# Kernel optimization log

Hardware: AMD Instinct MI355X
Metric: run time of the kernel (lower is better)

## Reference

```python
import jax, jax.numpy as jnp
import numpy as np

B, N, F, H, D = 4096, 14, 768, 1, 768  # batch, num_diseases, feature_dim, num_heads, hidden_dim
L = 3  # number of GAT layers


def setup_inputs() -> dict:
    key = jax.random.key(0)
    ks = jax.random.split(key, 8)
    features = jax.random.normal(ks[0], (B, N, F), dtype=jnp.float32)
    # random adjacency mask; ensure nonzero diagonal so no row is fully masked
    mask = (jax.random.uniform(ks[1], (B, N, N)) > 0.3).astype(jnp.float32)
    adj = jnp.maximum(mask, jnp.eye(N, dtype=jnp.float32))
    W_emb = jax.random.normal(ks[2], (F, D), dtype=jnp.float32) / np.sqrt(F)
    b_emb = jnp.zeros((D,), dtype=jnp.float32)
    gat_W = jax.random.normal(ks[3], (L, D, H * D), dtype=jnp.float32) / np.sqrt(D)
    gat_a = jax.random.normal(ks[4], (L, 2 * D, H), dtype=jnp.float32) / np.sqrt(2 * D)
    W_out = jax.random.normal(ks[5], (H * D, F), dtype=jnp.float32) / np.sqrt(H * D)
    b_out = jnp.zeros((F,), dtype=jnp.float32)
    return dict(features=features, adj=adj, W_emb=W_emb, b_emb=b_emb,
                gat_W=gat_W, gat_a=gat_a, W_out=W_out, b_out=b_out)


def _gat_layer(x, adj, W, a):
    # x: [B, N, D], W: [D, H*D], a: [2D, H]
    Bm, Nn = x.shape[0], x.shape[1]
    Wh = (x @ W).reshape(Bm, Nn, H, D)
    # e[b,i,j,h] = Wh[b,i,h] . a[:D,h] + Wh[b,j,h] . a[D:,h]  (concat attention, un-materialized)
    a_i, a_j = a[:D], a[D:]
    ei = jnp.einsum('bnhd,dh->bnh', Wh, a_i)
    ej = jnp.einsum('bnhd,dh->bnh', Wh, a_j)
    e = ei[:, :, None, :] + ej[:, None, :, :]  # [B, N, N, H]
    e = jnp.where(adj[..., None] > 0, e, jnp.float32(-1e30))  # masked_fill(-inf)
    attn = jax.nn.softmax(e, axis=2)  # softmax over j (dim=2), matches torch
    h = jnp.einsum('bijh,bjhd->bihd', attn, Wh)  # attention-weighted aggregation
    return h.reshape(Bm, Nn, H * D), attn  # concat=True output


def reference(features, adj, W_emb, b_emb, gat_W, gat_a, W_out, b_out):
    # dropout layers are identity at inference
    x = features @ W_emb + b_emb  # disease_embedding
    attns = []
    for l in range(L):
        x, attn = _gat_layer(x, adj, gat_W[l], gat_a[l])
        attns.append(attn)
        if l < L - 1:
            x = jax.nn.elu(x)
    out = x @ W_out + b_out  # output_proj
    return (out, attns[0], attns[1], attns[2])
```

## Files before the change

### kernel.cpp

```cpp
#include <hip/hip_runtime.h>

typedef unsigned short u16;
typedef float f32x16 __attribute__((ext_vector_type(16)));
typedef short bf16x8 __attribute__((ext_vector_type(8)));
typedef unsigned short u16x8 __attribute__((ext_vector_type(8)));

#define ND 768
#define KD 768

__device__ __forceinline__ float bf2f(u16 u) {
    union { unsigned i; float f; } v; v.i = ((unsigned)u) << 16; return v.f;
}
__device__ __forceinline__ u16 f2bf(float f) {
    union { float f; unsigned u; } x; x.f = f;
    unsigned r = x.u + 0x7fffu + ((x.u >> 16) & 1u);
    return (u16)(r >> 16);
}
__device__ __forceinline__ void async16(const void* g, void* l) {
    __builtin_amdgcn_global_load_lds((const __attribute__((address_space(1))) void*)g,
                                     (__attribute__((address_space(3))) void*)l, 16, 0, 0);
}

__global__ __launch_bounds__(256) void conv_w(const float* __restrict__ W_emb,
                                              const float* __restrict__ gat_W,
                                              const float* __restrict__ W_out,
                                              u16* __restrict__ Wt)
{
    __shared__ float lds[64][65];
    const int m  = blockIdx.x / 144;
    const int r  = blockIdx.x % 144;
    const int tr = r / 12;
    const int tc = r % 12;
    const float* src = (m == 0) ? W_emb : (m <= 3) ? (gat_W + (size_t)(m - 1) * 589824) : W_out;
    const int c  = threadIdx.x & 63;
    const int w4 = threadIdx.x >> 6;
    #pragma unroll
    for (int i = 0; i < 16; ++i) {
        int kk = i * 4 + w4;
        lds[kk][c] = src[(size_t)(tr * 64 + kk) * 768 + tc * 64 + c];
    }
    __syncthreads();
    u16* dst = Wt + (size_t)m * 589824;
    #pragma unroll
    for (int i = 0; i < 16; ++i) {
        int nn = i * 4 + w4;
        dst[(size_t)(tc * 64 + nn) * 768 + tr * 64 + c] = f2bf(lds[c][nn]);
    }
}

__global__ __launch_bounds__(256) void conv_w2(const float* __restrict__ src0,
                                               u16* __restrict__ dst0)
{
    __shared__ float lds[64][65];
    const int m  = blockIdx.x / 144;
    const int r  = blockIdx.x % 144;
    const int tr = r / 12;
    const int tc = r % 12;
    const float* src = src0 + (size_t)m * 589824;
    u16* dst = dst0 + (size_t)m * 589824;
    const int c  = threadIdx.x & 63;
    const int w4 = threadIdx.x >> 6;
    #pragma unroll
    for (int i = 0; i < 16; ++i) {
        int kk = i * 4 + w4;
        lds[kk][c] = src[(size_t)(tr * 64 + kk) * 768 + tc * 64 + c];
    }
    __syncthreads();
    #pragma unroll
    for (int i = 0; i < 16; ++i) {
        int nn = i * 4 + w4;
        dst[(size_t)(tc * 64 + nn) * 768 + tr * 64 + c] = f2bf(lds[c][nn]);
    }
}

__global__ __launch_bounds__(256) void conv_x(const float4* __restrict__ in,
                                              u16* __restrict__ outp, int n4)
{
    for (int i = blockIdx.x * 256 + threadIdx.x; i < n4; i += gridDim.x * 256) {
        float4 v = in[i];
        union { u16 s[4]; uint2 u; } o;
        o.s[0] = f2bf(v.x); o.s[1] = f2bf(v.y); o.s[2] = f2bf(v.z); o.s[3] = f2bf(v.w);
        ((uint2*)outp)[i] = o.u;
    }
}

__global__ __launch_bounds__(256) void prep_vecs(const float* __restrict__ W3,
                                                 const float* __restrict__ ga2,
                                                 const float* __restrict__ be,
                                                 const u16* __restrict__ Wt1,
                                                 float* __restrict__ w3ai,
                                                 float* __restrict__ w3aj,
                                                 float* __restrict__ bfus)
{
    int d = blockIdx.x * 256 + threadIdx.x;
    if (d >= 768) return;
    const float* row = W3 + (size_t)d * 768;
    float ai = 0.f, aj = 0.f;
    for (int n = 0; n < 768; ++n) { float w = row[n]; ai += w * ga2[n]; aj += w * ga2[768 + n]; }
    w3ai[d] = ai; w3aj[d] = aj;
    const u16* wt = Wt1 + (size_t)d * 768;
    float bf = 0.f;
    for (int j = 0; j < 768; ++j) bf += be[j] * bf2f(wt[j]);
    bfus[d] = bf;
}

template<bool F32OUT, bool SWZ>
__global__ __launch_bounds__(256) void gemm_bt(const u16* __restrict__ A,
                                               const u16* __restrict__ Bt,
                                               const u16* __restrict__ Bt2,
                                               const float* __restrict__ bias,
                                               void* __restrict__ Cout)
{
    __shared__ u16 lds3[3][2][4096];
    const int tid  = threadIdx.x;
    const int lane = tid & 63;
    const int wvb  = tid & ~63;
    const int wm   = ((tid >> 7) & 1) * 64;
    const int wn   = ((tid >> 6) & 1) * 64;
    const int wg = blockIdx.x;
    const int id = SWZ ? ((wg & 7) * 336 + (wg >> 3)) : wg;
    const int tn = (id % 6) * 128;
    const int tm = (id / 6) * 128;
    const u16* BtU = (Bt2 != nullptr && tm >= 768) ? Bt2 : Bt;

    f32x16 acc[2][2] = {};

    const int r31 = lane & 31;
    const int l5  = lane >> 5;
    const int key = (r31 >> 1) & 3;

    const int row0 = tid >> 2;
    const int kc0  = (((tid & 3) ^ ((tid >> 3) & 3)) << 3);
    const u16* aSrc = A   + (size_t)(tm + row0) * KD + kc0;
    const u16* bSrc = BtU + (size_t)(tn + row0) * KD + kc0;

    #define STAGE(b, ks_) { const int k0 = (ks_) * 32;                       \
        async16(aSrc + k0,                   &lds3[b][0][wvb * 8]);          \
        async16(aSrc + (size_t)64 * KD + k0, &lds3[b][0][(256 + wvb) * 8]);  \
        async16(bSrc + k0,                   &lds3[b][1][wvb * 8]);          \
        async16(bSrc + (size_t)64 * KD + k0, &lds3[b][1][(256 + wvb) * 8]); }

    STAGE(0, 0);
    STAGE(1, 1);

    #pragma unroll 3
    for (int ks = 0; ks < KD / 32; ++ks) {
        const int cur = ks % 3;
        if (ks < KD / 32 - 1)
            asm volatile("s_waitcnt vmcnt(4)" ::: "memory");
        else
            asm volatile("s_waitcnt vmcnt(0)" ::: "memory");
        __builtin_amdgcn_s_barrier();
        asm volatile("" ::: "memory");
        if (ks + 2 < KD / 32) STAGE((ks + 2) % 3, ks + 2);

        const u16* As = lds3[cur][0];
        const u16* Bs = lds3[cur][1];
        bf16x8 af[2][2], bf[2][2];
        #pragma unroll
        for (int fr = 0; fr < 2; ++fr)
            #pragma unroll
            for (int ka = 0; ka < 2; ++ka) {
                int chA = ((ka * 2 + l5) ^ key) << 3;
                af[fr][ka] = *(const bf16x8*)&As[(wm + fr * 32 + r31) * 32 + chA];
                bf[fr][ka] = *(const bf16x8*)&Bs[(wn + fr * 32 + r31) * 32 + chA];
            }
        #pragma unroll
        for (int fr = 0; fr < 2; ++fr)
            #pragma unroll
            for (int fc = 0; fc < 2; ++fc)
                #pragma unroll
                for (int ka = 0; ka < 2; ++ka)
                    acc[fr][fc] = __builtin_amdgcn_mfma_f32_32x32x16_bf16(
                        af[fr][ka], bf[fc][ka], acc[fr][fc], 0, 0, 0);
    }
    #undef STAGE

    #pragma unroll
    for (int fc = 0; fc < 2; ++fc) {
        int col = tn + wn + fc * 32 + r31;
        float bv = bias ? bias[col] : 0.0f;
        #pragma unroll
        for (int fr = 0; fr < 2; ++fr) {
            int rowb = tm + wm + fr * 32 + 4 * l5;
            #pragma unroll
            for (int reg = 0; reg < 16; ++reg) {
                int row = rowb + (reg & 3) + 8 * (reg >> 2);
                float v = acc[fr][fc][reg] + bv;
                if (F32OUT)
                    ((float*)Cout)[(size_t)row * ND + col] = v;
                else
                    ((u16*)Cout)[(size_t)row * ND + col] = f2bf(v);
            }
        }
    }
}

template<bool ELU, bool DOTS>
__global__ __launch_bounds__(256) void gat_mix(const u16* __restrict__ Wh,
                                               const float* __restrict__ adj,
                                               const float* __restrict__ avec,
                                               float* __restrict__ attn_out,
                                               u16* __restrict__ Xout,
                                               const float* __restrict__ w3ai,
                                               const float* __restrict__ w3aj,
                                               float* __restrict__ eiOut,
                                               float* __restrict__ ejOut)
{
    __shared__ u16 wh[14 * 768];
    __shared__ float s_ei[14], s_ej[14];
    __shared__ float s_attn[196];
    __shared__ float s_dots[14][2];
    const int b = blockIdx.x;
    const int tid = threadIdx.x;
    const u16* whb = Wh + (size_t)b * 10752;

    if (DOTS && tid < 28) ((float*)s_dots)[tid] = 0.f;
    for (int c = tid; c < 1344; c += 256)
        ((uint4*)wh)[c] = ((const uint4*)whb)[c];
    __syncthreads();

    if (tid < 224) {
        const int i = tid >> 4, l = tid & 15;
        float ai = 0.f, aj = 0.f;
        #pragma unroll
        for (int c = 0; c < 6; ++c) {
            int d = c * 128 + l * 8;
            u16x8 v  = *(const u16x8*)&wh[i * 768 + d];
            float4 x0 = *(const float4*)&avec[d];
            float4 x1 = *(const float4*)&avec[d + 4];
            float4 y0 = *(const float4*)&avec[768 + d];
            float4 y1 = *(const float4*)&avec[768 + d + 4];
            float w0 = bf2f(v[0]), w1 = bf2f(v[1]), w2 = bf2f(v[2]), w3 = bf2f(v[3]);
            float w4 = bf2f(v[4]), w5 = bf2f(v[5]), w6 = bf2f(v[6]), w7 = bf2f(v[7]);
            ai += w0*x0.x + w1*x0.y + w2*x0.z + w3*x0.w + w4*x1.x + w5*x1.y + w6*x1.z + w7*x1.w;
            aj += w0*y0.x + w1*y0.y + w2*y0.z + w3*y0.w + w4*y1.x + w5*y1.y + w6*y1.z + w7*y1.w;
        }
        #pragma unroll
        for (int off = 8; off; off >>= 1) {
            ai += __shfl_xor(ai, off);
            aj += __shfl_xor(aj, off);
        }
        if (l == 0) { s_ei[i] = ai; s_ej[i] = aj; }
    }
    __syncthreads();

    if (tid < 14) {
        const int i = tid;
        float e[14];
        float mx = -3.0e38f;
        #pragma unroll
        for (int j = 0; j < 14; ++j) {
            float ev = (adj[(size_t)b * 196 + i * 14 + j] > 0.f) ? (s_ei[i] + s_ej[j]) : -1.0e30f;
            e[j] = ev; mx = fmaxf(mx, ev);
        }
        float sum = 0.f;
        #pragma unroll
        for (int j = 0; j < 14; ++j) { float pp = __expf(e[j] - mx); e[j] = pp; sum += pp; }
        float inv = 1.0f / sum;
        #pragma unroll
        for (int j = 0; j < 14; ++j) s_attn[i * 14 + j] = e[j] * inv;
    }
    __syncthreads();

    if (tid < 196) attn_out[(size_t)b * 196 + tid] = s_attn[tid];

    for (int pp = tid; pp < 14 * 48; pp += 256) {
        const int i  = pp / 48;
        const int d0 = (pp % 48) * 16;
        float acc[16] = {};
        #pragma unroll
        for (int j = 0; j < 14; ++j) {
            float aw = s_attn[i * 14 + j];
            u16x8 wv0 = *(const u16x8*)&wh[j * 768 + d0];
            u16x8 wv1 = *(const u16x8*)&wh[j * 768 + d0 + 8];
            #pragma unroll
            for (int qq = 0; qq < 8; ++qq) {
                acc[qq]     += aw * bf2f(wv0[qq]);
                acc[8 + qq] += aw * bf2f(wv1[qq]);
            }
        }
        float pi = 0.f, pj = 0.f;
        union { u16 s[16]; uint4 u[2]; } o;
        #pragma unroll
        for (int qq = 0; qq < 16; ++qq) {
            float v = acc[qq];
            if (ELU && v < 0.f) v = __expf(v) - 1.0f;
            if (DOTS) { pi += v * w3ai[d0 + qq]; pj += v * w3aj[d0 + qq]; }
            o.s[qq] = f2bf(v);
        }
        if (DOTS) {
            atomicAdd(&s_dots[i][0], pi);
            atomicAdd(&s_dots[i][1], pj);
        }
        *(uint4*)&Xout[(size_t)b * 10752 + i * 768 + d0]     = o.u[0];
        *(uint4*)&Xout[(size_t)b * 10752 + i * 768 + d0 + 8] = o.u[1];
    }
    if (DOTS) {
        __syncthreads();
        if (tid < 14) {
            eiOut[(size_t)b * 14 + tid] = s_dots[tid][0];
            ejOut[(size_t)b * 14 + tid] = s_dots[tid][1];
        }
    }
}

__global__ __launch_bounds__(256) void gat_out(const u16* __restrict__ Z,
                                               const float* __restrict__ adj,
                                               const float* __restrict__ eiG,
                                               const float* __restrict__ ejG,
                                               const float* __restrict__ b_out,
                                               float* __restrict__ attn_out,
                                               float* __restrict__ outp)
{
    __shared__ u16 wh[14 * 768];
    __shared__ float s_attn[196];
    const int b = blockIdx.x;
    const int tid = threadIdx.x;
    const u16* zb = Z + (size_t)b * 10752;

    for (int c = tid; c < 1344; c += 256)
        ((uint4*)wh)[c] = ((const uint4*)zb)[c];

    if (tid < 14) {
        const int i = tid;
        float ei = eiG[(size_t)b * 14 + i];
        float e[14];
        float mx = -3.0e38f;
        #pragma unroll
        for (int j = 0; j < 14; ++j) {
            float ev = (adj[(size_t)b * 196 + i * 14 + j] > 0.f)
                           ? (ei + ejG[(size_t)b * 14 + j]) : -1.0e30f;
            e[j] = ev; mx = fmaxf(mx, ev);
        }
        float sum = 0.f;
        #pragma unroll
        for (int j = 0; j < 14; ++j) { float pp = __expf(e[j] - mx); e[j] = pp; sum += pp; }
        float inv = 1.0f / sum;
        #pragma unroll
        for (int j = 0; j < 14; ++j) s_attn[i * 14 + j] = e[j] * inv;
    }
    __syncthreads();

    if (tid < 196) attn_out[(size_t)b * 196 + tid] = s_attn[tid];

    for (int pp = tid; pp < 14 * 48; pp += 256) {
        const int i  = pp / 48;
        const int d0 = (pp % 48) * 16;
        float acc[16];
        #pragma unroll
        for (int qq = 0; qq < 16; ++qq) acc[qq] = b_out[d0 + qq];
        #pragma unroll
        for (int j = 0; j < 14; ++j) {
            float aw = s_attn[i * 14 + j];
            u16x8 wv0 = *(const u16x8*)&wh[j * 768 + d0];
            u16x8 wv1 = *(const u16x8*)&wh[j * 768 + d0 + 8];
            #pragma unroll
            for (int qq = 0; qq < 8; ++qq) {
                acc[qq]     += aw * bf2f(wv0[qq]);
                acc[8 + qq] += aw * bf2f(wv1[qq]);
            }
        }
        float* dst = &outp[(size_t)b * 10752 + i * 768 + d0];
        *(float4*)(dst)      = *(float4*)&acc[0];
        *(float4*)(dst + 4)  = *(float4*)&acc[4];
        *(float4*)(dst + 8)  = *(float4*)&acc[8];
        *(float4*)(dst + 12) = *(float4*)&acc[12];
    }
}

extern "C" void kernel_launch(void* const* d_in, const int* in_sizes, int n_in,
                              void* d_out, int out_size, void* d_ws, size_t ws_size,
                              hipStream_t stream)
{
    const float* features = (const float*)d_in[0];
    const float* adj      = (const float*)d_in[1];
    const float* W_emb    = (const float*)d_in[2];
    const float* b_emb    = (const float*)d_in[3];
    const float* gat_W    = (const float*)d_in[4];
    const float* gat_a    = (const float*)d_in[5];
    const float* W_out    = (const float*)d_in[6];
    const float* b_out    = (const float*)d_in[7];
    float* out = (float*)d_out;

    u16* Wh = (u16*)d_ws;
    u16* Wt = Wh + 44040192;
    float* scr  = (float*)(Wt + 7 * 589824);
    float* w3ai = scr + 1179648;
    float* w3aj = w3ai + 768;
    float* bfus = w3aj + 768;
    float* eiG  = bfus + 768;
    float* ejG  = eiG + 57344;
    u16* H0 = (u16*)d_out;
    u16* H1 = H0 + 44040192;
    u16* WeW3 = H1;
    float* attn0 = out + 44040192;
    float* attn1 = attn0 + 802816;
    float* attn2 = attn1 + 802816;

    conv_w<<<dim3(720), 256, 0, stream>>>(W_emb, gat_W, W_out, Wt);
    conv_x<<<dim3(4096), 256, 0, stream>>>((const float4*)features, H0, 11010048);
    conv_x<<<dim3(576), 256, 0, stream>>>((const float4*)W_emb, WeW3, 147456);
    conv_x<<<dim3(576), 256, 0, stream>>>((const float4*)(gat_W + 2 * 589824), WeW3 + 589824, 147456);
    prep_vecs<<<dim3(3), 256, 0, stream>>>(gat_W + 2 * 589824, gat_a + 2 * 1536, b_emb,
                                           Wt + 589824, w3ai, w3aj, bfus);
    gemm_bt<true, false><<<dim3(72), 256, 0, stream>>>(
        WeW3, Wt + 1 * 589824, Wt + 4 * 589824, nullptr, scr);
    conv_w2<<<dim3(288), 256, 0, stream>>>(scr, Wt + 5 * 589824);

    dim3 gg(2688);
    gemm_bt<false, true><<<gg, 256, 0, stream>>>(
        H0, Wt + 5 * 589824, nullptr, bfus, Wh);
    gat_mix<true, false><<<dim3(4096), 256, 0, stream>>>(Wh, adj, gat_a, attn0, H1,
                                                         nullptr, nullptr, nullptr, nullptr);
    gemm_bt<false, true><<<gg, 256, 0, stream>>>(
        H1, Wt + 2 * 589824, nullptr, nullptr, Wh);
    gat_mix<true, true><<<dim3(4096), 256, 0, stream>>>(Wh, adj, gat_a + 1536, attn1, H0,
                                                        w3ai, w3aj, eiG, ejG);
    gemm_bt<false, true><<<gg, 256, 0, stream>>>(
        H0, Wt + 6 * 589824, nullptr, nullptr, Wh);
    gat_out<<<dim3(4096), 256, 0, stream>>>(Wh, adj, eiG, ejG, b_out, attn2, out);
}
```

Before: 638.6 us.

## Merge weight prep kernels, parallelize prep_vecs, emit fused weights pre-transposed

Merges the weight transposes, the bf16 casts of W_emb and W3, and the features cast into one mega_prep launch. prep_vecs now gives one wavefront per output row with a shuffle reduction instead of one serial thread per row. The small fused-weight GEMM swaps operand roles so its bf16 output is already transposed, which removes the fp32 scratch buffer and the conv_w2 transpose. These cut launch count and serial prep latency, at the cost of a more branchy prep kernel and a skipped W_emb transpose slot.

```diff
diff --git a/kernel.cpp b/kernel.cpp
--- a/kernel.cpp
+++ b/kernel.cpp
@@ -21,91 +21,89 @@
                                      (__attribute__((address_space(3))) void*)l, 16, 0, 0);
 }
 
-__global__ __launch_bounds__(256) void conv_w(const float* __restrict__ W_emb,
-                                              const float* __restrict__ gat_W,
-                                              const float* __restrict__ W_out,
-                                              u16* __restrict__ Wt)
+__global__ __launch_bounds__(256) void mega_prep(const float* __restrict__ W_emb,
+                                                 const float* __restrict__ gat_W,
+                                                 const float* __restrict__ W_out,
+                                                 const float4* __restrict__ features,
+                                                 u16* __restrict__ Wt,
+                                                 u16* __restrict__ WeBf,
+                                                 u16* __restrict__ W3Bf,
+                                                 u16* __restrict__ H0)
 {
     __shared__ float lds[64][65];
-    const int m  = blockIdx.x / 144;
-    const int r  = blockIdx.x % 144;
-    const int tr = r / 12;
-    const int tc = r % 12;
-    const float* src = (m == 0) ? W_emb : (m <= 3) ? (gat_W + (size_t)(m - 1) * 589824) : W_out;
-    const int c  = threadIdx.x & 63;
-    const int w4 = threadIdx.x >> 6;
-    #pragma unroll
-    for (int i = 0; i < 16; ++i) {
-        int kk = i * 4 + w4;
-        lds[kk][c] = src[(size_t)(tr * 64 + kk) * 768 + tc * 64 + c];
-    }
-    __syncthreads();
-    u16* dst = Wt + (size_t)m * 589824;
-    #pragma unroll
-    for (int i = 0; i < 16; ++i) {
-        int nn = i * 4 + w4;
-        dst[(size_t)(tc * 64 + nn) * 768 + tr * 64 + c] = f2bf(lds[c][nn]);
-    }
-}
-
-__global__ __launch_bounds__(256) void conv_w2(const float* __restrict__ src0,
-                                               u16* __restrict__ dst0)
-{
-    __shared__ float lds[64][65];
-    const int m  = blockIdx.x / 144;
-    const int r  = blockIdx.x % 144;
-    const int tr = r / 12;
-    const int tc = r % 12;
-    const float* src = src0 + (size_t)m * 589824;
-    u16* dst = dst0 + (size_t)m * 589824;
-    const int c  = threadIdx.x & 63;
-    const int w4 = threadIdx.x >> 6;
-    #pragma unroll
-    for (int i = 0; i < 16; ++i) {
-        int kk = i * 4 + w4;
-        lds[kk][c] = src[(size_t)(tr * 64 + kk) * 768 + tc * 64 + c];
-    }
-    __syncthreads();
-    #pragma unroll
-    for (int i = 0; i < 16; ++i) {
-        int nn = i * 4 + w4;
-        dst[(size_t)(tc * 64 + nn) * 768 + tr * 64 + c] = f2bf(lds[c][nn]);
-    }
-}
-
-__global__ __launch_bounds__(256) void conv_x(const float4* __restrict__ in,
-                                              u16* __restrict__ outp, int n4)
-{
-    for (int i = blockIdx.x * 256 + threadIdx.x; i < n4; i += gridDim.x * 256) {
-        float4 v = in[i];
+    const int blk = blockIdx.x;
+    const int tid = threadIdx.x;
+    if (blk < 432) {
+        const int mi = blk / 144;
+        const int mm = (mi == 0) ? 1 : (mi == 1) ? 2 : 4;
+        const float* src = (mm == 4) ? W_out : gat_W + (size_t)(mm - 1) * 589824;
+        const int r  = blk % 144;
+        const int tr = r / 12, tc = r % 12;
+        const int c  = tid & 63, w4 = tid >> 6;
+        #pragma unroll
+        for (int i = 0; i < 16; ++i) {
+            int kk = i * 4 + w4;
+            lds[kk][c] = src[(size_t)(tr * 64 + kk) * 768 + tc * 64 + c];
+        }
+        __syncthreads();
+        u16* dst = Wt + (size_t)mm * 589824;
+        #pragma unroll
+        for (int i = 0; i < 16; ++i) {
+            int nn = i * 4 + w4;
+            dst[(size_t)(tc * 64 + nn) * 768 + tr * 64 + c] = f2bf(lds[c][nn]);
+        }
+    } else if (blk < 1584) {
+        int bi = blk - 432;
+        const float4* src;
+        u16* dst;
+        if (bi < 576) { src = (const float4*)W_emb; dst = WeBf; }
+        else          { src = (const float4*)(gat_W + 2 * 589824); dst = W3Bf; bi -= 576; }
+        const int i = bi * 256 + tid;
+        float4 v = src[i];
         union { u16 s[4]; uint2 u; } o;
         o.s[0] = f2bf(v.x); o.s[1] = f2bf(v.y); o.s[2] = f2bf(v.z); o.s[3] = f2bf(v.w);
-        ((uint2*)outp)[i] = o.u;
-    }
-}
-
-__global__ __launch_bounds__(256) void prep_vecs(const float* __restrict__ W3,
-                                                 const float* __restrict__ ga2,
-                                                 const float* __restrict__ be,
-                                                 const u16* __restrict__ Wt1,
-                                                 float* __restrict__ w3ai,
-                                                 float* __restrict__ w3aj,
-                                                 float* __restrict__ bfus)
-{
-    int d = blockIdx.x * 256 + threadIdx.x;
-    if (d >= 768) return;
+        ((uint2*)dst)[i] = o.u;
+    } else {
+        for (int i = (blk - 1584) * 256 + tid; i < 11010048; i += 4096 * 256) {
+            float4 v = features[i];
+            union { u16 s[4]; uint2 u; } o;
+            o.s[0] = f2bf(v.x); o.s[1] = f2bf(v.y); o.s[2] = f2bf(v.z); o.s[3] = f2bf(v.w);
+            ((uint2*)H0)[i] = o.u;
+        }
+    }
+}
+
+__global__ __launch_bounds__(256) void prep_vecs2(const float* __restrict__ W3,
+                                                  const float* __restrict__ ga2,
+                                                  const float* __restrict__ be,
+                                                  const u16* __restrict__ Wt1,
+                                                  float* __restrict__ w3ai,
+                                                  float* __restrict__ w3aj,
+                                                  float* __restrict__ bfus)
+{
+    const int lane = threadIdx.x & 63;
+    const int d = blockIdx.x * 4 + (threadIdx.x >> 6);
     const float* row = W3 + (size_t)d * 768;
-    float ai = 0.f, aj = 0.f;
-    for (int n = 0; n < 768; ++n) { float w = row[n]; ai += w * ga2[n]; aj += w * ga2[768 + n]; }
-    w3ai[d] = ai; w3aj[d] = aj;
-    const u16* wt = Wt1 + (size_t)d * 768;
-    float bf = 0.f;
-    for (int j = 0; j < 768; ++j) bf += be[j] * bf2f(wt[j]);
-    bfus[d] = bf;
+    const u16* wrow = Wt1 + (size_t)d * 768;
+    float ai = 0.f, aj = 0.f, bf = 0.f;
+    for (int j = lane; j < 768; j += 64) {
+        float w = row[j];
+        ai += w * ga2[j];
+        aj += w * ga2[768 + j];
+        bf += be[j] * bf2f(wrow[j]);
+    }
+    #pragma unroll
+    for (int off = 32; off; off >>= 1) {
+        ai += __shfl_down(ai, off);
+        aj += __shfl_down(aj, off);
+        bf += __shfl_down(bf, off);
+    }
+    if (lane == 0) { w3ai[d] = ai; w3aj[d] = aj; bfus[d] = bf; }
 }
 
 template<bool F32OUT, bool SWZ>
 __global__ __launch_bounds__(256) void gemm_bt(const u16* __restrict__ A,
+                                               const u16* __restrict__ A2,
                                                const u16* __restrict__ Bt,
                                                const u16* __restrict__ Bt2,
                                                const float* __restrict__ bias,
@@ -121,7 +119,10 @@
     const int id = SWZ ? ((wg & 7) * 336 + (wg >> 3)) : wg;
     const int tn = (id % 6) * 128;
     const int tm = (id / 6) * 128;
-    const u16* BtU = (Bt2 != nullptr && tm >= 768) ? Bt2 : Bt;
+    const bool hi = (A2 != nullptr) && (tm >= 768);
+    const u16* AU  = hi ? A2 : A;
+    const u16* BtU = hi ? Bt2 : Bt;
+    const int tmA  = hi ? tm - 768 : tm;
 
     f32x16 acc[2][2] = {};
 
@@ -131,7 +132,7 @@
 
     const int row0 = tid >> 2;
     const int kc0  = (((tid & 3) ^ ((tid >> 3) & 3)) << 3);
-    const u16* aSrc = A   + (size_t)(tm + row0) * KD + kc0;
+    const u16* aSrc = AU  + (size_t)(tmA + row0) * KD + kc0;
     const u16* bSrc = BtU + (size_t)(tn + row0) * KD + kc0;
 
     #define STAGE(b, ks_) { const int k0 = (ks_) * 32;                       \
@@ -385,39 +386,37 @@
 
     u16* Wh = (u16*)d_ws;
     u16* Wt = Wh + 44040192;
-    float* scr  = (float*)(Wt + 7 * 589824);
-    float* w3ai = scr + 1179648;
+    float* w3ai = (float*)(Wt + 7 * 589824);
     float* w3aj = w3ai + 768;
     float* bfus = w3aj + 768;
     float* eiG  = bfus + 768;
     float* ejG  = eiG + 57344;
     u16* H0 = (u16*)d_out;
     u16* H1 = H0 + 44040192;
-    u16* WeW3 = H1;
+    u16* WeBf = H1;
+    u16* W3Bf = H1 + 589824;
     float* attn0 = out + 44040192;
     float* attn1 = attn0 + 802816;
     float* attn2 = attn1 + 802816;
 
-    conv_w<<<dim3(720), 256, 0, stream>>>(W_emb, gat_W, W_out, Wt);
-    conv_x<<<dim3(4096), 256, 0, stream>>>((const float4*)features, H0, 11010048);
-    conv_x<<<dim3(576), 256, 0, stream>>>((const float4*)W_emb, WeW3, 147456);
-    conv_x<<<dim3(576), 256, 0, stream>>>((const float4*)(gat_W + 2 * 589824), WeW3 + 589824, 147456);
-    prep_vecs<<<dim3(3), 256, 0, stream>>>(gat_W + 2 * 589824, gat_a + 2 * 1536, b_emb,
-                                           Wt + 589824, w3ai, w3aj, bfus);
-    gemm_bt<true, false><<<dim3(72), 256, 0, stream>>>(
-        WeW3, Wt + 1 * 589824, Wt + 4 * 589824, nullptr, scr);
-    conv_w2<<<dim3(288), 256, 0, stream>>>(scr, Wt + 5 * 589824);
+    mega_prep<<<dim3(5680), 256, 0, stream>>>(W_emb, gat_W, W_out,
+                                              (const float4*)features,
+                                              Wt, WeBf, W3Bf, H0);
+    prep_vecs2<<<dim3(192), 256, 0, stream>>>(gat_W + 2 * 589824, gat_a + 2 * 1536, b_emb,
+                                              Wt + 589824, w3ai, w3aj, bfus);
+    gemm_bt<false, false><<<dim3(72), 256, 0, stream>>>(
+        Wt + 1 * 589824, Wt + 4 * 589824, WeBf, W3Bf, nullptr, Wt + 5 * 589824);
 
     dim3 gg(2688);
     gemm_bt<false, true><<<gg, 256, 0, stream>>>(
-        H0, Wt + 5 * 589824, nullptr, bfus, Wh);
+        H0, nullptr, Wt + 5 * 589824, nullptr, bfus, Wh);
     gat_mix<true, false><<<dim3(4096), 256, 0, stream>>>(Wh, adj, gat_a, attn0, H1,
                                                          nullptr, nullptr, nullptr, nullptr);
     gemm_bt<false, true><<<gg, 256, 0, stream>>>(
-        H1, Wt + 2 * 589824, nullptr, nullptr, Wh);
+        H1, nullptr, Wt + 2 * 589824, nullptr, nullptr, Wh);
     gat_mix<true, true><<<dim3(4096), 256, 0, stream>>>(Wh, adj, gat_a + 1536, attn1, H0,
                                                         w3ai, w3aj, eiG, ejG);
     gemm_bt<false, true><<<gg, 256, 0, stream>>>(
-        H0, Wt + 6 * 589824, nullptr, nullptr, Wh);
+        H0, nullptr, Wt + 6 * 589824, nullptr, nullptr, Wh);
     gat_out<<<dim3(4096), 256, 0, stream>>>(Wh, adj, eiG, ejG, b_out, attn2, out);
 }
```

Result: faster. 593.8 us (-7.0%).
